# Optimization experiments

Hardware: AMD Instinct MI355X
Metric: run time of the kernel (lower is better)

## Reference

```python
import jax, jax.numpy as jnp
import numpy as np

EPS = 1e-6


def setup_inputs() -> dict:
    key = jax.random.key(0)
    k1, k2, k3 = jax.random.split(key, 3)
    B, J, V = 8, 17, 64
    coord_volumes_batch = jax.random.normal(k1, (B, V, V, V, 3), dtype=jnp.float32)
    volumes_batch_pred = jax.random.uniform(k2, (B, J, V, V, V), dtype=jnp.float32)
    keypoints_gt = jax.random.normal(k3, (B, J, 3), dtype=jnp.float32)
    keypoints_binary_validity = jnp.ones((B, J, 1), dtype=jnp.float32)
    return {
        "coord_volumes_batch": coord_volumes_batch,
        "volumes_batch_pred": volumes_batch_pred,
        "keypoints_gt": keypoints_gt,
        "keypoints_binary_validity": keypoints_binary_validity,
    }


def reference(coord_volumes_batch, volumes_batch_pred, keypoints_gt, keypoints_binary_validity):
    B, J = volumes_batch_pred.shape[:2]
    # Flatten the voxel grid: [B, N, 3] with N = X*Y*Z
    coord_flat = coord_volumes_batch.reshape(B, 1, -1, 3)          # [B, 1, N, 3]
    kp = keypoints_gt[:, :, None, :]                               # [B, J, 1, 3]
    # Squared distance per voxel; argmin of d^2 == argmin of sqrt(d^2)
    d2 = jnp.sum((coord_flat - kp) ** 2, axis=-1)                  # [B, J, N]
    min_idx = jnp.argmin(d2, axis=-1)                              # [B, J] flat voxel index
    pred_flat = volumes_batch_pred.reshape(B, J, -1)               # [B, J, N]
    p = jnp.take_along_axis(pred_flat, min_idx[..., None], axis=-1)[..., 0]  # [B, J]
    validity = keypoints_binary_validity[..., 0]                   # [B, J]
    loss = jnp.sum(validity * -jnp.log(p + EPS))
    n_losses = B * J  # original counts every (batch, joint) pair regardless of validity
    return loss / n_losses
```

## Files before the change

kernel.cpp:

```cpp
#include <hip/hip_runtime.h>

#define BATCH 8
#define NJ 17
#define NBJ (BATCH*NJ)
#define NV3 (64*64*64)
#define VPT 8
#define BLOCK 256
#define CHUNKS (NV3 / (BLOCK * VPT))
#define EPSV 1e-6f

__global__ __launch_bounds__(BLOCK) void vce_argmin_kernel(
    const float* __restrict__ coord,
    const float* __restrict__ kp,
    unsigned long long* __restrict__ part)
{
    const int blk   = blockIdx.x;
    const int b     = blk / CHUNKS;
    const int chunk = blk % CHUNKS;
    const int t     = threadIdx.x;
    const int lane  = t & 63;
    const int wave  = t >> 6;

    const int v0 = chunk * (BLOCK * VPT) + t * VPT;
    const float4* cp = (const float4*)(coord + (size_t)b * NV3 * 3 + (size_t)v0 * 3);
    float v[24];
#pragma unroll
    for (int i = 0; i < 6; ++i) {
        const float4 c = cp[i];
        v[4*i+0] = c.x; v[4*i+1] = c.y; v[4*i+2] = c.z; v[4*i+3] = c.w;
    }

    float vv[VPT];
#pragma unroll
    for (int k = 0; k < VPT; ++k)
        vv[k] = fmaf(v[3*k], v[3*k], fmaf(v[3*k+1], v[3*k+1], v[3*k+2]*v[3*k+2]));

    const float* kpb = kp + (size_t)b * NJ * 3;

    __shared__ unsigned long long red[BLOCK/64][NJ];

#pragma unroll
    for (int j = 0; j < NJ; ++j) {
        const float kx = kpb[3*j+0];
        const float ky = kpb[3*j+1];
        const float kz = kpb[3*j+2];

        float best = 3.4e38f;
        unsigned int bi = 0u;
#pragma unroll
        for (int k = 0; k < VPT; ++k) {
            const float dot   = fmaf(v[3*k], kx, fmaf(v[3*k+1], ky, v[3*k+2]*kz));
            const float score = fmaf(-2.0f, dot, vv[k]);
            if (score < best) { best = score; bi = (unsigned int)(v0 + k); }
        }

        float m = best;
#pragma unroll
        for (int off = 1; off < 64; off <<= 1)
            m = fminf(m, __shfl_xor(m, off, 64));

        const unsigned long long mask = __ballot(best == m);
        const int fl = __ffsll(mask) - 1;
        const unsigned int fbi = __shfl(bi, fl, 64);

        if (lane == 0) {
            unsigned int sb = __float_as_uint(m);
            sb ^= ((unsigned int)((int)sb >> 31)) | 0x80000000u;
            red[wave][j] = ((unsigned long long)sb << 32) | (unsigned long long)fbi;
        }
    }
    __syncthreads();

    if (t < NJ) {
        unsigned long long p = red[0][t];
#pragma unroll
        for (int w = 1; w < BLOCK/64; ++w) {
            const unsigned long long q = red[w][t];
            if (q < p) p = q;
        }
        part[(size_t)(b * NJ + t) * CHUNKS + chunk] = p;
    }
}

#define BLOCK2 576
__global__ __launch_bounds__(BLOCK2) void vce_loss_kernel(
    const float* __restrict__ pred,
    const float* __restrict__ validity,
    const unsigned long long* __restrict__ part,
    float* __restrict__ out)
{
    const int t  = threadIdx.x;
    const int bj = t >> 2;
    const int s  = t & 3;

    __shared__ float arr[NBJ];

    if (bj < NBJ) {
        unsigned long long m = ~0ull;
        const unsigned long long* p = part + (size_t)bj * CHUNKS;
#pragma unroll
        for (int i = 0; i < CHUNKS/4; ++i) {
            const unsigned long long q = p[s + 4*i];
            if (q < m) m = q;
        }
#pragma unroll
        for (int off = 1; off <= 2; off <<= 1) {
            const unsigned long long q = __shfl_xor(m, off, 64);
            if (q < m) m = q;
        }
        if (s == 0) {
            const unsigned int idx = (unsigned int)(m & 0xFFFFFFFFull);
            const float pv = pred[(size_t)bj * NV3 + idx];
            arr[bj] = validity[bj] * (-logf(pv + EPSV));
        }
    }
    __syncthreads();

    if (t < 64) {
        float x = arr[t] + arr[t + 64] + ((t < NBJ - 128) ? arr[t + 128] : 0.0f);
#pragma unroll
        for (int off = 32; off > 0; off >>= 1)
            x += __shfl_down(x, off, 64);
        if (t == 0) out[0] = x / (float)NBJ;
    }
}

extern "C" void kernel_launch(void* const* d_in, const int* in_sizes, int n_in,
                              void* d_out, int out_size, void* d_ws, size_t ws_size,
                              hipStream_t stream) {
    const float* coord    = (const float*)d_in[0];
    const float* pred     = (const float*)d_in[1];
    const float* kp       = (const float*)d_in[2];
    const float* validity = (const float*)d_in[3];
    float* out = (float*)d_out;
    unsigned long long* part = (unsigned long long*)d_ws;

    vce_argmin_kernel<<<BATCH * CHUNKS, BLOCK, 0, stream>>>(coord, kp, part);
    vce_loss_kernel<<<1, BLOCK2, 0, stream>>>(pred, validity, part, out);
}
```

Before: 20.42 us.

## Fuse argmin and loss kernels with last-block atomic counter, double voxels per thread

Merges the two launches into one kernel. Each block publishes its partial argmin, then increments a global atomic counter, and the last block to finish does the final reduction, the gather and the loss. Voxels per thread go from 8 to 16, which halves the grid and the number of partials the last block must scan. It adds a memset launch and a serial tail in one block, and the larger per-thread register footprint may lower occupancy.

```diff
diff --git a/kernel.cpp b/kernel.cpp
--- a/kernel.cpp
+++ b/kernel.cpp
@@ -4,15 +4,20 @@
 #define NJ 17
 #define NBJ (BATCH*NJ)
 #define NV3 (64*64*64)
-#define VPT 8
+#define VPT 16
 #define BLOCK 256
 #define CHUNKS (NV3 / (BLOCK * VPT))
+#define GRID (BATCH * CHUNKS)
 #define EPSV 1e-6f
 
-__global__ __launch_bounds__(BLOCK) void vce_argmin_kernel(
+__global__ __launch_bounds__(BLOCK) void vce_fused_kernel(
     const float* __restrict__ coord,
+    const float* __restrict__ pred,
     const float* __restrict__ kp,
-    unsigned long long* __restrict__ part)
+    const float* __restrict__ validity,
+    unsigned long long* __restrict__ part,
+    unsigned int* __restrict__ counter,
+    float* __restrict__ out)
 {
     const int blk   = blockIdx.x;
     const int b     = blk / CHUNKS;
@@ -23,9 +28,9 @@
 
     const int v0 = chunk * (BLOCK * VPT) + t * VPT;
     const float4* cp = (const float4*)(coord + (size_t)b * NV3 * 3 + (size_t)v0 * 3);
-    float v[24];
+    float v[3 * VPT];
 #pragma unroll
-    for (int i = 0; i < 6; ++i) {
+    for (int i = 0; i < 3 * VPT / 4; ++i) {
         const float4 c = cp[i];
         v[4*i+0] = c.x; v[4*i+1] = c.y; v[4*i+2] = c.z; v[4*i+3] = c.w;
     }
@@ -60,7 +65,7 @@
             m = fminf(m, __shfl_xor(m, off, 64));
 
         const unsigned long long mask = __ballot(best == m);
-        const int fl = __ffsll(mask) - 1;
+        const int fl = __ffsll((long long)mask) - 1;
         const unsigned int fbi = __shfl(bi, fl, 64);
 
         if (lane == 0) {
@@ -80,39 +85,30 @@
         }
         part[(size_t)(b * NJ + t) * CHUNKS + chunk] = p;
     }
-}
 
-#define BLOCK2 576
-__global__ __launch_bounds__(BLOCK2) void vce_loss_kernel(
-    const float* __restrict__ pred,
-    const float* __restrict__ validity,
-    const unsigned long long* __restrict__ part,
-    float* __restrict__ out)
-{
-    const int t  = threadIdx.x;
-    const int bj = t >> 2;
-    const int s  = t & 3;
+    __threadfence();
+    __shared__ unsigned int rank;
+    if (t == 0)
+        rank = __hip_atomic_fetch_add(counter, 1u, __ATOMIC_ACQ_REL,
+                                      __HIP_MEMORY_SCOPE_AGENT);
+    __syncthreads();
+    if (rank != GRID - 1) return;
+
+    __threadfence();
 
     __shared__ float arr[NBJ];
-
-    if (bj < NBJ) {
+    if (t < NBJ) {
         unsigned long long m = ~0ull;
-        const unsigned long long* p = part + (size_t)bj * CHUNKS;
-#pragma unroll
-        for (int i = 0; i < CHUNKS/4; ++i) {
-            const unsigned long long q = p[s + 4*i];
+        const unsigned long long* p = part + (size_t)t * CHUNKS;
+#pragma unroll 8
+        for (int i = 0; i < CHUNKS; ++i) {
+            const unsigned long long q = __hip_atomic_load(
+                (unsigned long long*)&p[i], __ATOMIC_RELAXED, __HIP_MEMORY_SCOPE_AGENT);
             if (q < m) m = q;
         }
-#pragma unroll
-        for (int off = 1; off <= 2; off <<= 1) {
-            const unsigned long long q = __shfl_xor(m, off, 64);
-            if (q < m) m = q;
-        }
-        if (s == 0) {
-            const unsigned int idx = (unsigned int)(m & 0xFFFFFFFFull);
-            const float pv = pred[(size_t)bj * NV3 + idx];
-            arr[bj] = validity[bj] * (-logf(pv + EPSV));
-        }
+        const unsigned int idx = (unsigned int)(m & 0xFFFFFFFFull);
+        const float pv = pred[(size_t)t * NV3 + idx];
+        arr[t] = validity[t] * (-logf(pv + EPSV));
     }
     __syncthreads();
 
@@ -133,8 +129,11 @@
     const float* kp       = (const float*)d_in[2];
     const float* validity = (const float*)d_in[3];
     float* out = (float*)d_out;
+
     unsigned long long* part = (unsigned long long*)d_ws;
+    unsigned int* counter = (unsigned int*)((char*)d_ws + (size_t)NBJ * CHUNKS * 8);
 
-    vce_argmin_kernel<<<BATCH * CHUNKS, BLOCK, 0, stream>>>(coord, kp, part);
-    vce_loss_kernel<<<1, BLOCK2, 0, stream>>>(pred, validity, part, out);
+    hipMemsetAsync(counter, 0, sizeof(unsigned int), stream);
+    vce_fused_kernel<<<GRID, BLOCK, 0, stream>>>(coord, pred, kp, validity,
+                                                 part, counter, out);
 }
```

Result: slower. 70.53 us (+245.4%).
